# Optimization experiments

Measured on AMD Instinct MI355X. Metric: run time of the kernel, lower is better.

## Reference

```python
import jax, jax.numpy as jnp
import numpy as np

B, S, E, H, K = 64, 512, 256, 512, 100


def setup_inputs() -> dict:
    key = jax.random.key(0)
    ks = jax.random.split(key, 7)
    scale = 0.02
    return {
        "event_types": jax.random.randint(ks[0], (B, S), 0, K),
        "time_deltas": jax.random.uniform(ks[1], (B, S), dtype=jnp.float32),
        "embedding": jax.random.normal(ks[2], (K, E), dtype=jnp.float32) * scale,
        "W": jax.random.normal(ks[3], (E + H, 5 * H), dtype=jnp.float32) * scale,
        "b": jnp.zeros((5 * H,), dtype=jnp.float32),
        "Wi": jax.random.normal(ks[4], (H, K), dtype=jnp.float32) * scale,
        "bi": jnp.zeros((K,), dtype=jnp.float32),
    }


def _ctlstm_scan(x_seq, dt_seq, W, b, hidden_dim):
    """x_seq: [B,S,E], dt_seq: [B,S]. Returns h_seq [B,S,H], decay_seq [B,S,H]."""
    bsz = x_seq.shape[0]
    h0 = jnp.zeros((bsz, hidden_dim), x_seq.dtype)
    c0 = jnp.zeros((bsz, hidden_dim), x_seq.dtype)

    def step(carry, inp):
        h, c = carry
        x_t, dt_t = inp  # [B,E], [B]
        z = jnp.concatenate([x_t, h], axis=-1) @ W + b  # [B,5H]
        i, f, o, g, d = jnp.split(z, 5, axis=-1)
        i = jax.nn.sigmoid(i)
        f = jax.nn.sigmoid(f)
        o = jax.nn.sigmoid(o)
        g = jnp.tanh(g)
        decay = jax.nn.softplus(d)  # decay rate >= 0
        c_new = f * c + i * g
        c_t = c_new * jnp.exp(-decay * dt_t[:, None])  # continuous-time decay
        h_t = o * jnp.tanh(c_t)
        return (h_t, c_t), (h_t, decay)

    # time-major for scan
    xs = (jnp.swapaxes(x_seq, 0, 1), jnp.swapaxes(dt_seq, 0, 1))
    _, (h_seq, decay_seq) = jax.lax.scan(step, (h0, c0), xs)
    return jnp.swapaxes(h_seq, 0, 1), jnp.swapaxes(decay_seq, 0, 1)


def reference(event_types, time_deltas, embedding, W, b, Wi, bi):
    x_seq = embedding[event_types]  # [B,S,E]
    hidden_state, decay_rate = _ctlstm_scan(x_seq, time_deltas, W, b, H)
    base_intensities = jax.nn.softplus(hidden_state @ Wi + bi)  # [B,S,K]
    return hidden_state, decay_rate, base_intensities
```

## Files before the change

kernel.cpp:

```cpp
#include <hip/hip_runtime.h>
#include <hip/hip_bf16.h>
#include <stdint.h>

#define BB 64
#define SS 512
#define EE 256
#define HH 512
#define NWG 32

typedef short s16x8 __attribute__((ext_vector_type(8)));
typedef float vf4 __attribute__((ext_vector_type(4)));

#define OFF_WBT   0UL
#define OFF_EMB   3932160UL
#define OFF_WIT   3983360UL
#define OFF_DTT   4098048UL
#define OFF_FLAGS 4229120UL
#define OFF_HBUF  4491264UL
#define OFF_ZXP   38045696UL

__device__ __forceinline__ int fidx(int t, int w, int v) {
  return (((t >> 4) * 128) + w * 4 + v) * 16 + (t & 15);
}

__device__ __forceinline__ unsigned short f2bf(float f) {
  unsigned u = __float_as_uint(f);
  u += 0x7fffu + ((u >> 16) & 1u);
  return (unsigned short)(u >> 16);
}
__device__ __forceinline__ float bf2f(unsigned short h) {
  return __uint_as_float(((unsigned)h) << 16);
}
__device__ __forceinline__ float sigmoidf_(float x) { return 1.f / (1.f + __expf(-x)); }
__device__ __forceinline__ float softplusf_(float x) {
  return fmaxf(x, 0.f) + log1pf(__expf(-fabsf(x)));
}
__device__ __forceinline__ float tanhf_(float x) {
  float e = __expf(2.f * x);
  return 1.f - 2.f / (e + 1.f);
}

__global__ void init_kernel(const float* __restrict__ W, const float* __restrict__ emb,
                            const float* __restrict__ Wi, const float* __restrict__ td,
                            unsigned short* __restrict__ WbT, unsigned short* __restrict__ embB,
                            unsigned short* __restrict__ WiT, float* __restrict__ dtT,
                            int* __restrict__ flags) {
  unsigned i = blockIdx.x * 256u + threadIdx.x;
  if (i < 1966080u) {
    unsigned c = i / 768u, k = i % 768u;
    WbT[i] = f2bf(W[(size_t)k * 2560u + c]);
    return;
  }
  i -= 1966080u;
  if (i < 25600u) { embB[i] = f2bf(emb[i]); return; }
  i -= 25600u;
  if (i < 57344u) {
    unsigned c = i / 512u, k = i % 512u;
    WiT[i] = f2bf(c < 100u ? Wi[(size_t)k * 100u + c] : 0.f);
    return;
  }
  i -= 57344u;
  if (i < 32768u) {
    unsigned t = i / 64u, b = i % 64u;
    dtT[i] = td[(size_t)b * 512u + t];
    return;
  }
  i -= 32768u;
  if (i < 65536u) { flags[i] = 0; return; }
}

__global__ __launch_bounds__(256, 2)
void zx_kernel(const int* __restrict__ evt, const unsigned short* __restrict__ embB,
               const unsigned short* __restrict__ WbT, const float* __restrict__ bias,
               unsigned short* __restrict__ zxp) {
  const int t = blockIdx.y;
  const int tid = threadIdx.x;
  const int v = tid >> 6, lane = tid & 63;
  const int m = lane & 15, quad = lane >> 4;
  const int cbase = blockIdx.x * 256 + v * 64;

  s16x8 Breg[8][4];
#pragma unroll
  for (int cf = 0; cf < 4; ++cf) {
    const unsigned short* bp = WbT + (size_t)(cbase + cf * 16 + m) * 768 + quad * 8;
#pragma unroll
    for (int ch = 0; ch < 8; ++ch) Breg[ch][cf] = *(const s16x8*)(bp + ch * 32);
  }
  int ev[4];
#pragma unroll
  for (int rt = 0; rt < 4; ++rt) ev[rt] = evt[(size_t)(rt * 16 + m) * 512 + t];

  vf4 acc[4][4];
#pragma unroll
  for (int cf = 0; cf < 4; ++cf) {
    float bbv = bias[cbase + cf * 16 + m];
#pragma unroll
    for (int rt = 0; rt < 4; ++rt) acc[rt][cf] = (vf4){bbv, bbv, bbv, bbv};
  }
#pragma unroll
  for (int ch = 0; ch < 8; ++ch) {
#pragma unroll
    for (int rt = 0; rt < 4; ++rt) {
      s16x8 a = *(const s16x8*)(embB + (size_t)ev[rt] * 256 + ch * 32 + quad * 8);
#pragma unroll
      for (int cf = 0; cf < 4; ++cf)
        acc[rt][cf] = __builtin_amdgcn_mfma_f32_16x16x32_bf16(a, Breg[ch][cf], acc[rt][cf], 0, 0, 0);
    }
  }
#pragma unroll
  for (int cf = 0; cf < 4; ++cf) {
    int col0 = cbase + cf * 16;
    int g = col0 >> 9;
    int w = (col0 & 511) >> 4;
#pragma unroll
    for (int rt = 0; rt < 4; ++rt) {
      unsigned h0 = f2bf(acc[rt][cf][0]);
      unsigned h1 = f2bf(acc[rt][cf][1]);
      unsigned h2 = f2bf(acc[rt][cf][2]);
      unsigned h3 = f2bf(acc[rt][cf][3]);
      uint2 val;
      val.x = h0 | (h1 << 16);
      val.y = h2 | (h3 << 16);
      ((uint2*)zxp)[((((size_t)t * 32 + w) * 4 + rt) * 5 + g) * 64 + lane] = val;
    }
  }
}

__global__ __launch_bounds__(256, 1)
void scan_kernel(const unsigned short* __restrict__ WbT,
                 const unsigned short* __restrict__ zxp,
                 const float* __restrict__ dtT,
                 unsigned short* __restrict__ hbuf,
                 int* __restrict__ flags,
                 float* __restrict__ out_h, float* __restrict__ out_d) {
  const int w = blockIdx.x;
  const int tid = threadIdx.x;
  const int v = tid >> 6, lane = tid & 63;
  const int m = lane & 15, quad = lane >> 4;
  const int rowb = v * 16;
  const int bb0 = rowb + quad * 4;
  const int col = w * 16 + m;

  s16x8 Breg[16][5];
#pragma unroll
  for (int g = 0; g < 5; ++g) {
    const unsigned short* bp = WbT + (size_t)(g * 512 + w * 16 + m) * 768 + 256 + quad * 8;
#pragma unroll
    for (int ch = 0; ch < 16; ++ch) Breg[ch][g] = *(const s16x8*)(bp + ch * 32);
  }

  vf4 cst = (vf4){0.f, 0.f, 0.f, 0.f};

  for (int t = 0; t < 512; ++t) {
    vf4 acc[5];
#pragma unroll
    for (int g = 0; g < 5; ++g) {
      uint2 zv = ((const uint2*)zxp)[((((size_t)t * 32 + w) * 4 + v) * 5 + g) * 64 + lane];
      acc[g][0] = bf2f((unsigned short)(zv.x & 0xffffu));
      acc[g][1] = bf2f((unsigned short)(zv.x >> 16));
      acc[g][2] = bf2f((unsigned short)(zv.y & 0xffffu));
      acc[g][3] = bf2f((unsigned short)(zv.y >> 16));
    }
    vf4 dt4 = *(const vf4*)(dtT + t * 64 + bb0);

    if (t > 0) {
      const int tp = t - 1;
      if (lane < 32) {
        const int* fp = flags + fidx(tp, lane, v);
        while (__hip_atomic_load(fp, __ATOMIC_RELAXED, __HIP_MEMORY_SCOPE_AGENT) == 0) {
          __builtin_amdgcn_s_sleep(1);
        }
      }
      __asm__ __volatile__("" ::: "memory");
      const unsigned short* hsrc =
          hbuf + (size_t)tp * (BB * HH) + (size_t)(rowb + m) * HH + quad * 8;
#pragma unroll
      for (int ch = 0; ch < 16; ++ch) {
        s16x8 a = *(const s16x8*)(hsrc + ch * 32);
#pragma unroll
        for (int g = 0; g < 5; ++g)
          acc[g] = __builtin_amdgcn_mfma_f32_16x16x32_bf16(a, Breg[ch][g], acc[g], 0, 0, 0);
      }
    }

    float hv[4], dv[4];
#pragma unroll
    for (int r = 0; r < 4; ++r) {
      float i_ = sigmoidf_(acc[0][r]);
      float f_ = sigmoidf_(acc[1][r]);
      float o_ = sigmoidf_(acc[2][r]);
      float g_ = tanhf_(acc[3][r]);
      float dec = softplusf_(acc[4][r]);
      float cn = f_ * cst[r] + i_ * g_;
      float ct = cn * __expf(-dec * dt4[r]);
      float h_ = o_ * tanhf_(ct);
      cst[r] = ct;
      hv[r] = h_; dv[r] = dec;
      __hip_atomic_store(hbuf + (size_t)t * (BB * HH) + (size_t)(bb0 + r) * HH + col,
                         f2bf(h_), __ATOMIC_RELAXED, __HIP_MEMORY_SCOPE_AGENT);
    }
    __asm__ __volatile__("" ::: "memory");
    __builtin_amdgcn_s_waitcnt(0);
    __asm__ __volatile__("" ::: "memory");
    if (lane == 0) {
      __hip_atomic_store(flags + fidx(t, w, v), 1, __ATOMIC_RELAXED,
                         __HIP_MEMORY_SCOPE_AGENT);
    }
#pragma unroll
    for (int r = 0; r < 4; ++r) {
      size_t oo = ((size_t)(bb0 + r) * SS + t) * HH + col;
      out_h[oo] = hv[r];
      out_d[oo] = dv[r];
    }
  }
}

__global__ __launch_bounds__(256, 2)
void inten_kernel(const unsigned short* __restrict__ hbuf,
                  const unsigned short* __restrict__ WiT,
                  const float* __restrict__ bi,
                  float* __restrict__ out_i) {
  const int b = blockIdx.y;
  const int t0 = blockIdx.x * 64;
  const int tid = threadIdx.x;
  const int v = tid >> 6, lane = tid & 63;
  const int m = lane & 15, quad = lane >> 4;
  const int trow = t0 + v * 16 + m;

  vf4 acc[7];
#pragma unroll
  for (int cf = 0; cf < 7; ++cf) {
    int c = cf * 16 + m;
    float bbv = (c < 100) ? bi[c] : 0.f;
    acc[cf] = (vf4){bbv, bbv, bbv, bbv};
  }
  const unsigned short* ha = hbuf + ((size_t)trow * 64 + b) * 512 + quad * 8;
#pragma unroll 4
  for (int ch = 0; ch < 16; ++ch) {
    s16x8 a = *(const s16x8*)(ha + ch * 32);
#pragma unroll
    for (int cf = 0; cf < 7; ++cf) {
      s16x8 bf = *(const s16x8*)(WiT + (size_t)(cf * 16 + m) * 512 + ch * 32 + quad * 8);
      acc[cf] = __builtin_amdgcn_mfma_f32_16x16x32_bf16(a, bf, acc[cf], 0, 0, 0);
    }
  }
#pragma unroll
  for (int cf = 0; cf < 7; ++cf) {
    int c = cf * 16 + m;
#pragma unroll
    for (int r = 0; r < 4; ++r) {
      int tt = t0 + v * 16 + quad * 4 + r;
      if (c < 100) out_i[((size_t)b * 512 + tt) * 100 + c] = softplusf_(acc[cf][r]);
    }
  }
}

extern "C" void kernel_launch(void* const* d_in, const int* in_sizes, int n_in,
                              void* d_out, int out_size, void* d_ws, size_t ws_size,
                              hipStream_t stream) {
  (void)in_sizes; (void)n_in; (void)out_size; (void)ws_size;
  const int*   evt  = (const int*)d_in[0];
  const float* td   = (const float*)d_in[1];
  const float* emb  = (const float*)d_in[2];
  const float* W    = (const float*)d_in[3];
  const float* bias = (const float*)d_in[4];
  const float* Wi   = (const float*)d_in[5];
  const float* bi   = (const float*)d_in[6];

  char* ws = (char*)d_ws;
  unsigned short* WbT  = (unsigned short*)(ws + OFF_WBT);
  unsigned short* embB = (unsigned short*)(ws + OFF_EMB);
  unsigned short* WiT  = (unsigned short*)(ws + OFF_WIT);
  float*          dtT  = (float*)(ws + OFF_DTT);
  int*            flags= (int*)(ws + OFF_FLAGS);
  unsigned short* hbuf = (unsigned short*)(ws + OFF_HBUF);
  unsigned short* zxp  = (unsigned short*)(ws + OFF_ZXP);

  float* out_h = (float*)d_out;
  float* out_d = out_h + (size_t)BB * SS * HH;
  float* out_i = out_d + (size_t)BB * SS * HH;

  init_kernel<<<8390, 256, 0, stream>>>(W, emb, Wi, td, WbT, embB, WiT, dtT, flags);
  zx_kernel<<<dim3(10, 512), 256, 0, stream>>>(evt, embB, WbT, bias, zxp);
  scan_kernel<<<NWG, 256, 0, stream>>>(WbT, zxp, dtT, hbuf, flags, out_h, out_d);
  inten_kernel<<<dim3(8, 64), 256, 0, stream>>>(hbuf, WiT, bi, out_i);
}
```

Before: 3.703 ms.

## Elect scan workgroups on a single XCD and use lighter-scope inter-block sync

```diff
diff --git a/kernel.cpp b/kernel.cpp
--- a/kernel.cpp
+++ b/kernel.cpp
@@ -19,6 +19,7 @@
 #define OFF_HBUF  4491264UL
 #define OFF_ZXP   38045696UL
 
+
 __device__ __forceinline__ int fidx(int t, int w, int v) {
   return (((t >> 4) * 128) + w * 4 + v) * 16 + (t & 15);
 }
@@ -44,7 +45,7 @@
                             const float* __restrict__ Wi, const float* __restrict__ td,
                             unsigned short* __restrict__ WbT, unsigned short* __restrict__ embB,
                             unsigned short* __restrict__ WiT, float* __restrict__ dtT,
-                            int* __restrict__ flags) {
+                            int* __restrict__ flags, int* __restrict__ ctrl) {
   unsigned i = blockIdx.x * 256u + threadIdx.x;
   if (i < 1966080u) {
     unsigned c = i / 768u, k = i % 768u;
@@ -67,6 +68,8 @@
   }
   i -= 32768u;
   if (i < 65536u) { flags[i] = 0; return; }
+  i -= 65536u;
+  if (i < 64u) { ctrl[i] = (i == 0u) ? -1 : 0; return; }
 }
 
 __global__ __launch_bounds__(256, 2)
@@ -126,16 +129,15 @@
   }
 }
 
-__global__ __launch_bounds__(256, 1)
-void scan_kernel(const unsigned short* __restrict__ WbT,
-                 const unsigned short* __restrict__ zxp,
-                 const float* __restrict__ dtT,
-                 unsigned short* __restrict__ hbuf,
-                 int* __restrict__ flags,
-                 float* __restrict__ out_h, float* __restrict__ out_d) {
-  const int w = blockIdx.x;
-  const int tid = threadIdx.x;
-  const int v = tid >> 6, lane = tid & 63;
+template<int FAST>
+__device__ __forceinline__
+void scan_loop(const int w, const int v, const int lane,
+               const unsigned short* __restrict__ WbT,
+               const unsigned short* __restrict__ zxp,
+               const float* __restrict__ dtT,
+               unsigned short* __restrict__ hbuf,
+               int* __restrict__ flags,
+               float* __restrict__ out_h, float* __restrict__ out_d) {
   const int m = lane & 15, quad = lane >> 4;
   const int rowb = v * 16;
   const int bb0 = rowb + quad * 4;
@@ -167,8 +169,24 @@
       const int tp = t - 1;
       if (lane < 32) {
         const int* fp = flags + fidx(tp, lane, v);
-        while (__hip_atomic_load(fp, __ATOMIC_RELAXED, __HIP_MEMORY_SCOPE_AGENT) == 0) {
-          __builtin_amdgcn_s_sleep(1);
+        if (FAST) {
+          int it = 0;
+          for (;;) {
+            int f;
+            if (it < 48) {
+              asm volatile("global_load_dword %0, %1, off sc0\n\ts_waitcnt vmcnt(0)"
+                           : "=&v"(f) : "v"(fp) : "memory");
+            } else {
+              f = __hip_atomic_load(fp, __ATOMIC_RELAXED, __HIP_MEMORY_SCOPE_AGENT);
+            }
+            if (f != 0) break;
+            __builtin_amdgcn_s_sleep(1);
+            ++it;
+          }
+        } else {
+          while (__hip_atomic_load(fp, __ATOMIC_RELAXED, __HIP_MEMORY_SCOPE_AGENT) == 0) {
+            __builtin_amdgcn_s_sleep(1);
+          }
         }
       }
       __asm__ __volatile__("" ::: "memory");
@@ -196,15 +214,21 @@
       float h_ = o_ * tanhf_(ct);
       cst[r] = ct;
       hv[r] = h_; dv[r] = dec;
-      __hip_atomic_store(hbuf + (size_t)t * (BB * HH) + (size_t)(bb0 + r) * HH + col,
-                         f2bf(h_), __ATOMIC_RELAXED, __HIP_MEMORY_SCOPE_AGENT);
+      unsigned short hb = f2bf(h_);
+      size_t hi = (size_t)t * (BB * HH) + (size_t)(bb0 + r) * HH + col;
+      if (FAST) hbuf[hi] = hb;
+      else __hip_atomic_store(hbuf + hi, hb, __ATOMIC_RELAXED, __HIP_MEMORY_SCOPE_AGENT);
     }
     __asm__ __volatile__("" ::: "memory");
     __builtin_amdgcn_s_waitcnt(0);
     __asm__ __volatile__("" ::: "memory");
     if (lane == 0) {
-      __hip_atomic_store(flags + fidx(t, w, v), 1, __ATOMIC_RELAXED,
-                         __HIP_MEMORY_SCOPE_AGENT);
+      if (FAST)
+        __hip_atomic_store(flags + fidx(t, w, v), 1, __ATOMIC_RELAXED,
+                           __HIP_MEMORY_SCOPE_WORKGROUP);
+      else
+        __hip_atomic_store(flags + fidx(t, w, v), 1, __ATOMIC_RELAXED,
+                           __HIP_MEMORY_SCOPE_AGENT);
     }
 #pragma unroll
     for (int r = 0; r < 4; ++r) {
@@ -213,6 +237,76 @@
       out_d[oo] = dv[r];
     }
   }
+}
+
+__global__ __launch_bounds__(256, 1)
+void scan_kernel(const unsigned short* __restrict__ WbT,
+                 const unsigned short* __restrict__ zxp,
+                 const float* __restrict__ dtT,
+                 unsigned short* __restrict__ hbuf,
+                 int* __restrict__ flags,
+                 int* __restrict__ ctrl,
+                 float* __restrict__ out_h, float* __restrict__ out_d) {
+  __shared__ int sh[2];
+  if (threadIdx.x == 0) {
+    int xcd;
+    asm volatile("s_getreg_b32 %0, hwreg(HW_REG_XCC_ID)" : "=s"(xcd));
+    xcd &= 0xf;
+    int expct = -1;
+    bool won = __hip_atomic_compare_exchange_strong(
+        ctrl + 0, &expct, xcd, __ATOMIC_RELAXED, __ATOMIC_RELAXED,
+        __HIP_MEMORY_SCOPE_AGENT);
+    int tgt = won ? xcd : expct;
+    int rank = -1;
+    if (xcd == tgt) {
+      int r = __hip_atomic_fetch_add(ctrl + 1, 1, __ATOMIC_RELAXED,
+                                     __HIP_MEMORY_SCOPE_AGENT);
+      if (r < NWG) rank = r;
+    }
+    if (rank < 0) {
+      unsigned long long t0 = __builtin_amdgcn_s_memrealtime();
+      for (;;) {
+        if (__hip_atomic_load(ctrl + 1, __ATOMIC_RELAXED, __HIP_MEMORY_SCOPE_AGENT) >= NWG)
+          break;
+        if (__builtin_amdgcn_s_memrealtime() - t0 > 300000ull) {
+          int r = __hip_atomic_fetch_add(ctrl + 1, 1, __ATOMIC_RELAXED,
+                                         __HIP_MEMORY_SCOPE_AGENT);
+          if (r < NWG) rank = r;
+          break;
+        }
+        __builtin_amdgcn_s_sleep(32);
+      }
+    }
+    int mode = 0;
+    if (rank >= 0) {
+      __hip_atomic_store(ctrl + 4 + rank, xcd, __ATOMIC_RELAXED, __HIP_MEMORY_SCOPE_AGENT);
+      __hip_atomic_fetch_add(ctrl + 2, 1, __ATOMIC_RELEASE, __HIP_MEMORY_SCOPE_AGENT);
+      if (rank == 0) {
+        while (__hip_atomic_load(ctrl + 2, __ATOMIC_ACQUIRE, __HIP_MEMORY_SCOPE_AGENT) < NWG)
+          __builtin_amdgcn_s_sleep(8);
+        int same = 1;
+        for (int i2 = 1; i2 < NWG; ++i2)
+          same &= (__hip_atomic_load(ctrl + 4 + i2, __ATOMIC_RELAXED,
+                                     __HIP_MEMORY_SCOPE_AGENT) == xcd);
+        mode = same ? 2 : 1;
+        __hip_atomic_store(ctrl + 3, mode, __ATOMIC_RELEASE, __HIP_MEMORY_SCOPE_AGENT);
+      } else {
+        while ((mode = __hip_atomic_load(ctrl + 3, __ATOMIC_ACQUIRE,
+                                         __HIP_MEMORY_SCOPE_AGENT)) == 0)
+          __builtin_amdgcn_s_sleep(8);
+      }
+    }
+    sh[0] = rank; sh[1] = mode;
+  }
+  __syncthreads();
+  const int rank = sh[0];
+  if (rank < 0) return;
+  const int mode = sh[1];
+  const int v = (int)(threadIdx.x >> 6), lane = (int)(threadIdx.x & 63);
+  if (mode == 2)
+    scan_loop<1>(rank, v, lane, WbT, zxp, dtT, hbuf, flags, out_h, out_d);
+  else
+    scan_loop<0>(rank, v, lane, WbT, zxp, dtT, hbuf, flags, out_h, out_d);
 }
 
 __global__ __launch_bounds__(256, 2)
@@ -279,9 +373,10 @@
   float* out_h = (float*)d_out;
   float* out_d = out_h + (size_t)BB * SS * HH;
   float* out_i = out_d + (size_t)BB * SS * HH;
-
-  init_kernel<<<8390, 256, 0, stream>>>(W, emb, Wi, td, WbT, embB, WiT, dtT, flags);
+  int*   ctrl  = (int*)out_i;
+
+  init_kernel<<<8390, 256, 0, stream>>>(W, emb, Wi, td, WbT, embB, WiT, dtT, flags, ctrl);
   zx_kernel<<<dim3(10, 512), 256, 0, stream>>>(evt, embB, WbT, bias, zxp);
-  scan_kernel<<<NWG, 256, 0, stream>>>(WbT, zxp, dtT, hbuf, flags, out_h, out_d);
+  scan_kernel<<<256, 256, 0, stream>>>(WbT, zxp, dtT, hbuf, flags, ctrl, out_h, out_d);
   inten_kernel<<<dim3(8, 64), 256, 0, stream>>>(hbuf, WiT, bi, out_i);
 }
```

Result: slower. 7.240 ms (+95.5%).

## Replace per-step flag handshake with sentinel-in-data polling of h buffer

Applied to the files above, without the earlier changes.

```diff
diff --git a/kernel.cpp b/kernel.cpp
--- a/kernel.cpp
+++ b/kernel.cpp
@@ -9,7 +9,8 @@
 #define NWG 32
 
 typedef short s16x8 __attribute__((ext_vector_type(8)));
-typedef float vf4 __attribute__((ext_vector_type(4)));
+typedef int   v4i   __attribute__((ext_vector_type(4)));
+typedef float vf4   __attribute__((ext_vector_type(4)));
 
 #define OFF_WBT   0UL
 #define OFF_EMB   3932160UL
@@ -19,10 +20,6 @@
 #define OFF_HBUF  4491264UL
 #define OFF_ZXP   38045696UL
 
-__device__ __forceinline__ int fidx(int t, int w, int v) {
-  return (((t >> 4) * 128) + w * 4 + v) * 16 + (t & 15);
-}
-
 __device__ __forceinline__ unsigned short f2bf(float f) {
   unsigned u = __float_as_uint(f);
   u += 0x7fffu + ((u >> 16) & 1u);
@@ -38,6 +35,9 @@
 __device__ __forceinline__ float tanhf_(float x) {
   float e = __expf(2.f * x);
   return 1.f - 2.f / (e + 1.f);
+}
+__device__ __forceinline__ unsigned haszero16(unsigned x) {
+  return (x - 0x00010001u) & ~x & 0x80008000u;
 }
 
 __global__ void init_kernel(const float* __restrict__ W, const float* __restrict__ emb,
@@ -131,7 +131,6 @@
                  const unsigned short* __restrict__ zxp,
                  const float* __restrict__ dtT,
                  unsigned short* __restrict__ hbuf,
-                 int* __restrict__ flags,
                  float* __restrict__ out_h, float* __restrict__ out_d) {
   const int w = blockIdx.x;
   const int tid = threadIdx.x;
@@ -152,6 +151,18 @@
   vf4 cst = (vf4){0.f, 0.f, 0.f, 0.f};
 
   for (int t = 0; t < 512; ++t) {
+    v4i areg[16];
+    const unsigned short* hsrc =
+        hbuf + (size_t)(t - 1) * (BB * HH) + (size_t)(rowb + m) * HH + quad * 8;
+    if (t > 0) {
+#pragma unroll
+      for (int ch = 0; ch < 16; ++ch) {
+        const unsigned short* ap = hsrc + ch * 32;
+        asm volatile("global_load_dwordx4 %0, %1, off sc0 sc1"
+                     : "=v"(areg[ch]) : "v"(ap) : "memory");
+      }
+    }
+
     vf4 acc[5];
 #pragma unroll
     for (int g = 0; g < 5; ++g) {
@@ -164,19 +175,47 @@
     vf4 dt4 = *(const vf4*)(dtT + t * 64 + bb0);
 
     if (t > 0) {
-      const int tp = t - 1;
-      if (lane < 32) {
-        const int* fp = flags + fidx(tp, lane, v);
-        while (__hip_atomic_load(fp, __ATOMIC_RELAXED, __HIP_MEMORY_SCOPE_AGENT) == 0) {
-          __builtin_amdgcn_s_sleep(1);
+      unsigned bad = 0xffffu;
+      int it = 0;
+      for (;;) {
+        asm volatile("s_waitcnt vmcnt(0)" ::: "memory");
+        __builtin_amdgcn_sched_barrier(0);
+#pragma unroll
+        for (int ch = 0; ch < 16; ++ch) {
+          if (bad & (1u << ch)) {
+            unsigned z = haszero16((unsigned)areg[ch][0]) | haszero16((unsigned)areg[ch][1]) |
+                         haszero16((unsigned)areg[ch][2]) | haszero16((unsigned)areg[ch][3]);
+            if (__all(z == 0u)) bad &= ~(1u << ch);
+          }
+        }
+        if (!bad) break;
+        ++it;
+        if (it < 4096) {
+#pragma unroll
+          for (int ch = 0; ch < 16; ++ch) {
+            if (bad & (1u << ch)) {
+              const unsigned short* ap = hsrc + ch * 32;
+              asm volatile("global_load_dwordx4 %0, %1, off sc0 sc1"
+                           : "=v"(areg[ch]) : "v"(ap) : "memory");
+            }
+          }
+        } else {
+#pragma unroll
+          for (int ch = 0; ch < 16; ++ch) {
+            if (bad & (1u << ch)) {
+              const int* ap = (const int*)(hsrc + ch * 32);
+#pragma unroll
+              for (int d = 0; d < 4; ++d)
+                areg[ch][d] = __hip_atomic_load(ap + d, __ATOMIC_RELAXED,
+                                                __HIP_MEMORY_SCOPE_AGENT);
+            }
+          }
         }
       }
-      __asm__ __volatile__("" ::: "memory");
-      const unsigned short* hsrc =
-          hbuf + (size_t)tp * (BB * HH) + (size_t)(rowb + m) * HH + quad * 8;
+      __builtin_amdgcn_sched_barrier(0);
 #pragma unroll
       for (int ch = 0; ch < 16; ++ch) {
-        s16x8 a = *(const s16x8*)(hsrc + ch * 32);
+        s16x8 a = __builtin_bit_cast(s16x8, areg[ch]);
 #pragma unroll
         for (int g = 0; g < 5; ++g)
           acc[g] = __builtin_amdgcn_mfma_f32_16x16x32_bf16(a, Breg[ch][g], acc[g], 0, 0, 0);
@@ -196,15 +235,10 @@
       float h_ = o_ * tanhf_(ct);
       cst[r] = ct;
       hv[r] = h_; dv[r] = dec;
+      unsigned short hb = f2bf(h_);
+      if ((hb & 0x7fffu) == 0u) hb |= 1u;
       __hip_atomic_store(hbuf + (size_t)t * (BB * HH) + (size_t)(bb0 + r) * HH + col,
-                         f2bf(h_), __ATOMIC_RELAXED, __HIP_MEMORY_SCOPE_AGENT);
-    }
-    __asm__ __volatile__("" ::: "memory");
-    __builtin_amdgcn_s_waitcnt(0);
-    __asm__ __volatile__("" ::: "memory");
-    if (lane == 0) {
-      __hip_atomic_store(flags + fidx(t, w, v), 1, __ATOMIC_RELAXED,
-                         __HIP_MEMORY_SCOPE_AGENT);
+                         hb, __ATOMIC_RELAXED, __HIP_MEMORY_SCOPE_AGENT);
     }
 #pragma unroll
     for (int r = 0; r < 4; ++r) {
@@ -280,8 +314,9 @@
   float* out_d = out_h + (size_t)BB * SS * HH;
   float* out_i = out_d + (size_t)BB * SS * HH;
 
-  init_kernel<<<8390, 256, 0, stream>>>(W, emb, Wi, td, WbT, embB, WiT, dtT, flags);
+  init_kernel<<<8388, 256, 0, stream>>>(W, emb, Wi, td, WbT, embB, WiT, dtT, flags);
+  hipMemsetAsync(hbuf, 0, (size_t)SS * BB * HH * sizeof(unsigned short), stream);
   zx_kernel<<<dim3(10, 512), 256, 0, stream>>>(evt, embB, WbT, bias, zxp);
-  scan_kernel<<<NWG, 256, 0, stream>>>(WbT, zxp, dtT, hbuf, flags, out_h, out_d);
+  scan_kernel<<<NWG, 256, 0, stream>>>(WbT, zxp, dtT, hbuf, out_h, out_d);
   inten_kernel<<<dim3(8, 64), 256, 0, stream>>>(hbuf, WiT, bi, out_i);
 }
```

New measurement: 4.128 ms. 11.5% more time.
